# Kernel tuning notes

Measured on AMD Instinct MI355X. Metric: run time of the kernel, lower is better.

The kernel has to match this reference:

```python
import jax, jax.numpy as jnp
import numpy as np

E = 500_000
N_GRAPHS = 1024
NODE_F = 9      # node_attr_sz_0 = 4 + 5
EDGE_F = 1      # edge_attr_sz_0
U_F = 16        # u_attr_sz_0
H = 512         # h_sz
OUT_F = 512     # edge_attr_sz_1
F_IN = EDGE_F + 2 * NODE_F + U_F  # 35


def setup_inputs() -> dict:
    key = jax.random.key(0)
    ks = jax.random.split(key, 9)
    src = jax.random.normal(ks[0], (E, NODE_F), dtype=jnp.float32)
    dest = jax.random.normal(ks[1], (E, NODE_F), dtype=jnp.float32)
    edge_attr = jax.random.normal(ks[2], (E, EDGE_F), dtype=jnp.float32)
    u = jax.random.normal(ks[3], (N_GRAPHS, U_F), dtype=jnp.float32)
    batch = jax.random.randint(ks[4], (E,), 0, N_GRAPHS, dtype=jnp.int64)
    # MLP params (torch Linear: y = x @ W.T + b). Store as [in, out] for einsum.
    lim1 = 1.0 / np.sqrt(F_IN)
    W1 = jax.random.uniform(ks[5], (F_IN, H), minval=-lim1, maxval=lim1, dtype=jnp.float32)
    b1 = jax.random.uniform(ks[6], (H,), minval=-lim1, maxval=lim1, dtype=jnp.float32)
    lim2 = 1.0 / np.sqrt(H)
    W2 = jax.random.uniform(ks[7], (H, OUT_F), minval=-lim2, maxval=lim2, dtype=jnp.float32)
    b2 = jax.random.uniform(ks[8], (OUT_F,), minval=-lim2, maxval=lim2, dtype=jnp.float32)
    return {"src": src, "dest": dest, "edge_attr": edge_attr, "u": u,
            "batch": batch, "W1": W1, "b1": b1, "W2": W2, "b2": b2}


def reference(src, dest, edge_attr, u, batch, W1, b1, W2, b2):
    # gather per-edge global features, concat, 2-layer MLP
    x = jnp.concatenate([src, dest, edge_attr, u[batch]], axis=1)  # [E, 35]
    h = jax.nn.relu(x @ W1 + b1)                                   # [E, 512]
    return h @ W2 + b2                                             # [E, 512]
```

## Files before the change

### kernel.cpp

```cpp
#include <hip/hip_runtime.h>
#include <hip/hip_bf16.h>


#define E_TOTAL   500000
#define H_SZ      512
#define OUT_SZ    512
#define K1        64
#define MT        64
#define XS_PAD    72

typedef __attribute__((ext_vector_type(8))) short bf16x8;
typedef __attribute__((ext_vector_type(4))) float f32x4;

union V8 { bf16x8 v; unsigned short s[8]; };

static __device__ __forceinline__ unsigned short f2b(float f) {
    __hip_bfloat16 h = __float2bfloat16(f);
    return *reinterpret_cast<unsigned short*>(&h);
}

static __device__ __forceinline__ int hidx(int m, int k) {
    int ku = (k >> 3) ^ (m & 7);
    return (m << 9) + (ku << 3) + (k & 7);
}

__global__ __launch_bounds__(256) void prep_weights(
        const float* __restrict__ W1, const float* __restrict__ W2,
        unsigned short* __restrict__ W2t, unsigned short* __restrict__ W1t) {
    int t = blockIdx.x * 256 + threadIdx.x;
    const int total2 = H_SZ * OUT_SZ;
    if (t < total2) {
        int k = t >> 9, n = t & 511;
        W2t[n * H_SZ + k] = f2b(W2[k * OUT_SZ + n]);
    } else {
        int t1 = t - total2;
        if (t1 < K1 * 512) {
            int k = t1 >> 9, n = t1 & 511;
            float v = (k < 35) ? W1[k * H_SZ + n] : 0.0f;
            W1t[n * K1 + k] = f2b(v);
        }
    }
}

__global__ __launch_bounds__(512) void edge_mlp(
        const float* __restrict__ gsrc, const float* __restrict__ gdst,
        const float* __restrict__ gea,  const float* __restrict__ gu,
        const int* __restrict__ gbatch,
        const float* __restrict__ b1,   const float* __restrict__ b2,
        const unsigned short* __restrict__ W1t,
        const unsigned short* __restrict__ W2t,
        float* __restrict__ out) {

    __shared__ unsigned short hs[MT * 512];
    unsigned short* xs = hs;

    const int tid  = threadIdx.x;
    const int e0   = blockIdx.x * MT;
    const int l    = tid & 63;
    const int w    = tid >> 6;
    const int l15  = l & 15;
    const int quad = l >> 4;

    {
        const int el = tid >> 3;
        const int s  = tid & 7;
        const int c0 = s << 3;
        const int e  = e0 + el;
        V8 vv;
        if (e < E_TOTAL) {
            const int b = gbatch[e] & 1023;
            #pragma unroll
            for (int j = 0; j < 8; ++j) {
                const int c = c0 + j;
                float v;
                if      (c < 9)   v = gsrc[e * 9 + c];
                else if (c < 18)  v = gdst[e * 9 + (c - 9)];
                else if (c == 18) v = gea[e];
                else if (c < 35)  v = gu[(b << 4) + (c - 19)];
                else              v = 0.0f;
                vv.s[j] = f2b(v);
            }
        } else {
            #pragma unroll
            for (int j = 0; j < 8; ++j) vv.s[j] = 0;
        }
        *reinterpret_cast<bf16x8*>(&xs[el * XS_PAD + c0]) = vv.v;
    }
    __syncthreads();

    f32x4 acc[4][4];
    #pragma unroll
    for (int mi = 0; mi < 4; ++mi)
        #pragma unroll
        for (int ni = 0; ni < 4; ++ni)
            acc[mi][ni] = (f32x4){0.f, 0.f, 0.f, 0.f};

    #pragma unroll
    for (int ks = 0; ks < 2; ++ks) {
        bf16x8 afr[4], bfr[4];
        #pragma unroll
        for (int mi = 0; mi < 4; ++mi)
            afr[mi] = *reinterpret_cast<const bf16x8*>(
                &xs[(mi * 16 + l15) * XS_PAD + ks * 32 + quad * 8]);
        #pragma unroll
        for (int ni = 0; ni < 4; ++ni)
            bfr[ni] = *reinterpret_cast<const bf16x8*>(
                &W1t[(w * 64 + ni * 16 + l15) * K1 + ks * 32 + quad * 8]);
        #pragma unroll
        for (int mi = 0; mi < 4; ++mi)
            #pragma unroll
            for (int ni = 0; ni < 4; ++ni)
                acc[mi][ni] = __builtin_amdgcn_mfma_f32_16x16x32_bf16(
                    afr[mi], bfr[ni], acc[mi][ni], 0, 0, 0);
    }
    __syncthreads();

    #pragma unroll
    for (int ni = 0; ni < 4; ++ni) {
        const int col = w * 64 + ni * 16 + l15;
        const float bv = b1[col];
        #pragma unroll
        for (int mi = 0; mi < 4; ++mi)
            #pragma unroll
            for (int r = 0; r < 4; ++r) {
                const int row = mi * 16 + quad * 4 + r;
                const float v = acc[mi][ni][r] + bv;
                hs[hidx(row, col)] = f2b(v > 0.f ? v : 0.f);
            }
    }
    __syncthreads();

    #pragma unroll
    for (int mi = 0; mi < 4; ++mi)
        #pragma unroll
        for (int ni = 0; ni < 4; ++ni)
            acc[mi][ni] = (f32x4){0.f, 0.f, 0.f, 0.f};

    const unsigned short* w2p = W2t + (w * 64 + l15) * H_SZ + quad * 8;

    #pragma unroll 4
    for (int k0 = 0; k0 < 16; ++k0) {
        bf16x8 afr[4], bfr[4];
        const int kk = k0 * 32 + quad * 8;
        #pragma unroll
        for (int mi = 0; mi < 4; ++mi)
            afr[mi] = *reinterpret_cast<const bf16x8*>(&hs[hidx(mi * 16 + l15, kk)]);
        #pragma unroll
        for (int ni = 0; ni < 4; ++ni)
            bfr[ni] = *reinterpret_cast<const bf16x8*>(&w2p[ni * (16 * H_SZ) + k0 * 32]);
        #pragma unroll
        for (int mi = 0; mi < 4; ++mi)
            #pragma unroll
            for (int ni = 0; ni < 4; ++ni)
                acc[mi][ni] = __builtin_amdgcn_mfma_f32_16x16x32_bf16(
                    afr[mi], bfr[ni], acc[mi][ni], 0, 0, 0);
    }

    #pragma unroll
    for (int ni = 0; ni < 4; ++ni) {
        const int col = w * 64 + ni * 16 + l15;
        const float bv = b2[col];
        #pragma unroll
        for (int mi = 0; mi < 4; ++mi)
            #pragma unroll
            for (int r = 0; r < 4; ++r) {
                const int e = e0 + mi * 16 + quad * 4 + r;
                if (e < E_TOTAL)
                    out[(size_t)e * OUT_SZ + col] = acc[mi][ni][r] + bv;
            }
    }
}

extern "C" void kernel_launch(void* const* d_in, const int* in_sizes, int n_in,
                              void* d_out, int out_size, void* d_ws, size_t ws_size,
                              hipStream_t stream) {
    const float* src   = (const float*)d_in[0];
    const float* dst   = (const float*)d_in[1];
    const float* eattr = (const float*)d_in[2];
    const float* u     = (const float*)d_in[3];
    const int*   batch = (const int*)d_in[4];
    const float* W1    = (const float*)d_in[5];
    const float* b1    = (const float*)d_in[6];
    const float* W2    = (const float*)d_in[7];
    const float* b2    = (const float*)d_in[8];
    float* out = (float*)d_out;

    unsigned short* W2t = (unsigned short*)d_ws;
    unsigned short* W1t = W2t + H_SZ * OUT_SZ;

    const int prep_total = H_SZ * OUT_SZ + 512 * K1;
    prep_weights<<<(prep_total + 255) / 256, 256, 0, stream>>>(W1, W2, W2t, W1t);

    const int nblk = (E_TOTAL + MT - 1) / MT;
    edge_mlp<<<nblk, 512, 0, stream>>>(src, dst, eattr, u, batch,
                                       b1, b2, W1t, W2t, out);
}
```

Measured before the change: 1.600 ms.

## Persistent edge MLP kernel with async global-to-LDS prefetch of next tile inputs

Turns the one-block-per-64-edge kernel into a persistent kernel with 512 blocks that loop over tiles. Each iteration issues global_load_lds for the next tile's gathered inputs (src, dest, edge_attr, u[batch]) while the second GEMM runs on the current tile, so input gather latency is hidden behind compute. Biases are hoisted into registers once per block, and padding columns read from a zeroed workspace word. The cost is fewer resident blocks and fp32 input staging in LDS with bf16 conversion at fragment load time. The 500 MB fp32 output write probably still dominates the runtime.

```diff
diff --git a/kernel.cpp b/kernel.cpp
--- a/kernel.cpp
+++ b/kernel.cpp
@@ -7,7 +7,8 @@
 #define OUT_SZ    512
 #define K1        64
 #define MT        64
-#define XS_PAD    72
+#define NT        ((E_TOTAL + MT - 1) / MT)
+#define NB        512
 
 typedef __attribute__((ext_vector_type(8))) short bf16x8;
 typedef __attribute__((ext_vector_type(4))) float f32x4;
@@ -24,10 +25,18 @@
     return (m << 9) + (ku << 3) + (k & 7);
 }
 
+static __device__ __forceinline__ void gl_lds4(const float* g, float* lds) {
+    __builtin_amdgcn_global_load_lds(
+        (const __attribute__((address_space(1))) void*)g,
+        (__attribute__((address_space(3))) void*)lds, 4, 0, 0);
+}
+
 __global__ __launch_bounds__(256) void prep_weights(
         const float* __restrict__ W1, const float* __restrict__ W2,
-        unsigned short* __restrict__ W2t, unsigned short* __restrict__ W1t) {
+        unsigned short* __restrict__ W2t, unsigned short* __restrict__ W1t,
+        float* __restrict__ zw) {
     int t = blockIdx.x * 256 + threadIdx.x;
+    if (t == 0) zw[0] = 0.0f;
     const int total2 = H_SZ * OUT_SZ;
     if (t < total2) {
         int k = t >> 9, n = t & 511;
@@ -42,132 +51,177 @@
     }
 }
 
-__global__ __launch_bounds__(512) void edge_mlp(
+__global__ __launch_bounds__(512, 4) void edge_mlp(
         const float* __restrict__ gsrc, const float* __restrict__ gdst,
         const float* __restrict__ gea,  const float* __restrict__ gu,
         const int* __restrict__ gbatch,
         const float* __restrict__ b1,   const float* __restrict__ b2,
         const unsigned short* __restrict__ W1t,
         const unsigned short* __restrict__ W2t,
+        const float* __restrict__ zw,
         float* __restrict__ out) {
 
     __shared__ unsigned short hs[MT * 512];
-    unsigned short* xs = hs;
+    __shared__ float xs[5 * 512];
 
     const int tid  = threadIdx.x;
-    const int e0   = blockIdx.x * MT;
     const int l    = tid & 63;
     const int w    = tid >> 6;
     const int l15  = l & 15;
     const int quad = l >> 4;
 
-    {
-        const int el = tid >> 3;
-        const int s  = tid & 7;
-        const int c0 = s << 3;
-        const int e  = e0 + el;
-        V8 vv;
-        if (e < E_TOTAL) {
-            const int b = gbatch[e] & 1023;
-            #pragma unroll
-            for (int j = 0; j < 8; ++j) {
-                const int c = c0 + j;
-                float v;
-                if      (c < 9)   v = gsrc[e * 9 + c];
-                else if (c < 18)  v = gdst[e * 9 + (c - 9)];
-                else if (c == 18) v = gea[e];
-                else if (c < 35)  v = gu[(b << 4) + (c - 19)];
-                else              v = 0.0f;
-                vv.s[j] = f2b(v);
-            }
-        } else {
-            #pragma unroll
-            for (int j = 0; j < 8; ++j) vv.s[j] = 0;
-        }
-        *reinterpret_cast<bf16x8*>(&xs[el * XS_PAD + c0]) = vv.v;
-    }
-    __syncthreads();
-
-    f32x4 acc[4][4];
-    #pragma unroll
-    for (int mi = 0; mi < 4; ++mi)
-        #pragma unroll
-        for (int ni = 0; ni < 4; ++ni)
-            acc[mi][ni] = (f32x4){0.f, 0.f, 0.f, 0.f};
-
-    #pragma unroll
-    for (int ks = 0; ks < 2; ++ks) {
-        bf16x8 afr[4], bfr[4];
-        #pragma unroll
-        for (int mi = 0; mi < 4; ++mi)
-            afr[mi] = *reinterpret_cast<const bf16x8*>(
-                &xs[(mi * 16 + l15) * XS_PAD + ks * 32 + quad * 8]);
-        #pragma unroll
-        for (int ni = 0; ni < 4; ++ni)
-            bfr[ni] = *reinterpret_cast<const bf16x8*>(
-                &W1t[(w * 64 + ni * 16 + l15) * K1 + ks * 32 + quad * 8]);
-        #pragma unroll
-        for (int mi = 0; mi < 4; ++mi)
-            #pragma unroll
-            for (int ni = 0; ni < 4; ++ni)
-                acc[mi][ni] = __builtin_amdgcn_mfma_f32_16x16x32_bf16(
-                    afr[mi], bfr[ni], acc[mi][ni], 0, 0, 0);
-    }
-    __syncthreads();
-
+    const int se  = (w << 3) + (l >> 3);
+    const int sc7 = l & 7;
+
+    float b1r[4], b2r[4];
     #pragma unroll
     for (int ni = 0; ni < 4; ++ni) {
-        const int col = w * 64 + ni * 16 + l15;
-        const float bv = b1[col];
+        const int col = (w << 6) + (ni << 4) + l15;
+        b1r[ni] = b1[col];
+        b2r[ni] = b2[col];
+    }
+
+    const unsigned short* w2p = W2t + ((w << 6) + l15) * H_SZ + (quad << 3);
+
+    int t = blockIdx.x;
+
+    {
+        const int e  = min(t * MT + se, E_TOTAL - 1);
+        const int bl = gbatch[e] & 1023;
+        #pragma unroll
+        for (int fb = 0; fb < 5; ++fb) {
+            const int c = (fb << 3) + sc7;
+            const float* g =
+                (c < 9)   ? gsrc + (size_t)e * 9 + c :
+                (c < 18)  ? gdst + (size_t)e * 9 + (c - 9) :
+                (c == 18) ? gea + e :
+                (c < 35)  ? gu + (bl << 4) + (c - 19) :
+                            zw;
+            gl_lds4(g, &xs[(fb << 9) + (w << 6)]);
+        }
+    }
+
+    for (; t < NT; t += NB) {
+        asm volatile("s_waitcnt vmcnt(0)" ::: "memory");
+        __syncthreads();
+
+        const int tn = t + NB;
+        const bool have_next = (tn < NT);
+        int e_n = 0, bl_n = 0;
+        if (have_next) {
+            e_n  = min(tn * MT + se, E_TOTAL - 1);
+            bl_n = gbatch[e_n] & 1023;
+        }
+
+        f32x4 acc[4][4];
         #pragma unroll
         for (int mi = 0; mi < 4; ++mi)
             #pragma unroll
-            for (int r = 0; r < 4; ++r) {
-                const int row = mi * 16 + quad * 4 + r;
-                const float v = acc[mi][ni][r] + bv;
-                hs[hidx(row, col)] = f2b(v > 0.f ? v : 0.f);
+            for (int ni = 0; ni < 4; ++ni)
+                acc[mi][ni] = (f32x4){0.f, 0.f, 0.f, 0.f};
+
+        #pragma unroll
+        for (int ks = 0; ks < 2; ++ks) {
+            bf16x8 afr[4], bfr[4];
+            const int k0 = (ks << 5) + (quad << 3);
+            const int fb = k0 >> 3;
+            #pragma unroll
+            for (int mi = 0; mi < 4; ++mi) {
+                V8 a;
+                if (ks == 0 || quad == 0) {
+                    const float* p = &xs[(fb << 9) + (((mi << 4) + l15) << 3)];
+                    const f32x4 lo = *reinterpret_cast<const f32x4*>(p);
+                    const f32x4 hi = *reinterpret_cast<const f32x4*>(p + 4);
+                    #pragma unroll
+                    for (int j = 0; j < 4; ++j) {
+                        a.s[j]     = f2b(lo[j]);
+                        a.s[4 + j] = f2b(hi[j]);
+                    }
+                } else {
+                    #pragma unroll
+                    for (int j = 0; j < 8; ++j) a.s[j] = 0;
+                }
+                afr[mi] = a.v;
             }
-    }
-    __syncthreads();
-
-    #pragma unroll
-    for (int mi = 0; mi < 4; ++mi)
-        #pragma unroll
-        for (int ni = 0; ni < 4; ++ni)
-            acc[mi][ni] = (f32x4){0.f, 0.f, 0.f, 0.f};
-
-    const unsigned short* w2p = W2t + (w * 64 + l15) * H_SZ + quad * 8;
-
-    #pragma unroll 4
-    for (int k0 = 0; k0 < 16; ++k0) {
-        bf16x8 afr[4], bfr[4];
-        const int kk = k0 * 32 + quad * 8;
+            #pragma unroll
+            for (int ni = 0; ni < 4; ++ni)
+                bfr[ni] = *reinterpret_cast<const bf16x8*>(
+                    &W1t[((w << 6) + (ni << 4) + l15) * K1 + k0]);
+            #pragma unroll
+            for (int mi = 0; mi < 4; ++mi)
+                #pragma unroll
+                for (int ni = 0; ni < 4; ++ni)
+                    acc[mi][ni] = __builtin_amdgcn_mfma_f32_16x16x32_bf16(
+                        afr[mi], bfr[ni], acc[mi][ni], 0, 0, 0);
+        }
+
+        #pragma unroll
+        for (int ni = 0; ni < 4; ++ni) {
+            const int col = (w << 6) + (ni << 4) + l15;
+            #pragma unroll
+            for (int mi = 0; mi < 4; ++mi)
+                #pragma unroll
+                for (int r = 0; r < 4; ++r) {
+                    const int row = (mi << 4) + (quad << 2) + r;
+                    const float v = acc[mi][ni][r] + b1r[ni];
+                    hs[hidx(row, col)] = f2b(v > 0.f ? v : 0.f);
+                }
+        }
+        __syncthreads();
+
+        if (have_next) {
+            #pragma unroll
+            for (int fb = 0; fb < 5; ++fb) {
+                const int c = (fb << 3) + sc7;
+                const float* g =
+                    (c < 9)   ? gsrc + (size_t)e_n * 9 + c :
+                    (c < 18)  ? gdst + (size_t)e_n * 9 + (c - 9) :
+                    (c == 18) ? gea + e_n :
+                    (c < 35)  ? gu + (bl_n << 4) + (c - 19) :
+                                zw;
+                gl_lds4(g, &xs[(fb << 9) + (w << 6)]);
+            }
+        }
+
         #pragma unroll
         for (int mi = 0; mi < 4; ++mi)
-            afr[mi] = *reinterpret_cast<const bf16x8*>(&hs[hidx(mi * 16 + l15, kk)]);
-        #pragma unroll
-        for (int ni = 0; ni < 4; ++ni)
-            bfr[ni] = *reinterpret_cast<const bf16x8*>(&w2p[ni * (16 * H_SZ) + k0 * 32]);
-        #pragma unroll
-        for (int mi = 0; mi < 4; ++mi)
-            #pragma unroll
-            for (int ni = 0; ni < 4; ++ni)
-                acc[mi][ni] = __builtin_amdgcn_mfma_f32_16x16x32_bf16(
-                    afr[mi], bfr[ni], acc[mi][ni], 0, 0, 0);
-    }
-
-    #pragma unroll
-    for (int ni = 0; ni < 4; ++ni) {
-        const int col = w * 64 + ni * 16 + l15;
-        const float bv = b2[col];
-        #pragma unroll
-        for (int mi = 0; mi < 4; ++mi)
-            #pragma unroll
-            for (int r = 0; r < 4; ++r) {
-                const int e = e0 + mi * 16 + quad * 4 + r;
-                if (e < E_TOTAL)
-                    out[(size_t)e * OUT_SZ + col] = acc[mi][ni][r] + bv;
-            }
+            #pragma unroll
+            for (int ni = 0; ni < 4; ++ni)
+                acc[mi][ni] = (f32x4){0.f, 0.f, 0.f, 0.f};
+
+        #pragma unroll 4
+        for (int k0 = 0; k0 < 16; ++k0) {
+            bf16x8 afr[4], bfr[4];
+            const int kk = (k0 << 5) + (quad << 3);
+            #pragma unroll
+            for (int mi = 0; mi < 4; ++mi)
+                afr[mi] = *reinterpret_cast<const bf16x8*>(
+                    &hs[hidx((mi << 4) + l15, kk)]);
+            #pragma unroll
+            for (int ni = 0; ni < 4; ++ni)
+                bfr[ni] = *reinterpret_cast<const bf16x8*>(
+                    &w2p[(ni << 4) * H_SZ + (k0 << 5)]);
+            #pragma unroll
+            for (int mi = 0; mi < 4; ++mi)
+                #pragma unroll
+                for (int ni = 0; ni < 4; ++ni)
+                    acc[mi][ni] = __builtin_amdgcn_mfma_f32_16x16x32_bf16(
+                        afr[mi], bfr[ni], acc[mi][ni], 0, 0, 0);
+        }
+
+        const int e0 = t * MT;
+        #pragma unroll
+        for (int ni = 0; ni < 4; ++ni) {
+            const int col = (w << 6) + (ni << 4) + l15;
+            #pragma unroll
+            for (int mi = 0; mi < 4; ++mi)
+                #pragma unroll
+                for (int r = 0; r < 4; ++r) {
+                    const int e = e0 + (mi << 4) + (quad << 2) + r;
+                    if (e < E_TOTAL)
+                        out[(size_t)e * OUT_SZ + col] = acc[mi][ni][r] + b2r[ni];
+                }
+        }
     }
 }
 
@@ -187,11 +241,11 @@
 
     unsigned short* W2t = (unsigned short*)d_ws;
     unsigned short* W1t = W2t + H_SZ * OUT_SZ;
+    float* zw = (float*)(W1t + 512 * K1);
 
     const int prep_total = H_SZ * OUT_SZ + 512 * K1;
-    prep_weights<<<(prep_total + 255) / 256, 256, 0, stream>>>(W1, W2, W2t, W1t);
-
-    const int nblk = (E_TOTAL + MT - 1) / MT;
-    edge_mlp<<<nblk, 512, 0, stream>>>(src, dst, eattr, u, batch,
-                                       b1, b2, W1t, W2t, out);
-}
+    prep_weights<<<(prep_total + 255) / 256, 256, 0, stream>>>(W1, W2, W2t, W1t, zw);
+
+    edge_mlp<<<NB, 512, 0, stream>>>(src, dst, eattr, u, batch,
+                                     b1, b2, W1t, W2t, zw, out);
+}
```

After: 1.756 ms. +9.7%, slower.
